# Kernel optimization log

Measured on AMD Instinct MI355X. Metric: run time of the kernel, lower is better.

## Reference

```python
import jax, jax.numpy as jnp
import numpy as np

B, S, D, DI = 8, 4096, 512, 2048
EPS = 1e-12  # torch F.normalize eps


def _l2norm(x):
    n = jnp.sqrt(jnp.sum(x * x, axis=-1, keepdims=True))
    return x / jnp.maximum(n, EPS)


def setup_inputs() -> dict:
    key = jax.random.key(0)
    ks = jax.random.split(key, 10)
    sd = 1.0 / np.sqrt(D)
    si = 1.0 / np.sqrt(DI)
    return {
        "x": jax.random.normal(ks[0], (B, S, D), jnp.float32),
        "wq": jax.random.uniform(ks[1], (D, DI), jnp.float32, -sd, sd),
        "wk": jax.random.uniform(ks[2], (D, DI), jnp.float32, -sd, sd),
        "wv": jax.random.uniform(ks[3], (D, DI), jnp.float32, -sd, sd),
        "wo": jax.random.uniform(ks[4], (DI, D), jnp.float32, -si, si),
        "w1": jax.random.uniform(ks[5], (D, DI), jnp.float32, -sd, sd),
        "b1": jax.random.uniform(ks[6], (DI,), jnp.float32, -sd, sd),
        "w2": jax.random.uniform(ks[7], (DI, D), jnp.float32, -si, si),
        "b2": jax.random.uniform(ks[8], (D,), jnp.float32, -si, si),
    }


def reference(x, wq, wk, wv, wo, w1, b1, w2, b2):
    # Hydra attention (linear): normalize(q) * sum_s(normalize(k)*v)
    q = _l2norm(jnp.einsum('bsd,de->bse', x, wq))
    k = _l2norm(jnp.einsum('bsd,de->bse', x, wk))
    v = jnp.einsum('bsd,de->bse', x, wv)
    kv = jnp.sum(k * v, axis=-2, keepdims=True)  # [B,1,DI]
    attn = jnp.einsum('bse,ed->bsd', q * kv, wo) + x  # dropout = identity (eval)
    # position-wise FFN with residual
    h = jax.nn.relu(jnp.einsum('bsd,de->bse', attn, w1) + b1)
    out = jnp.einsum('bse,ed->bsd', h, w2) + b2 + attn
    return out
```

## Files before the change

### kernel.cpp

```cpp
#include <hip/hip_runtime.h>
#include <stdint.h>

#define Bb  8
#define Ss  4096
#define Dd  512
#define DIi 2048
#define Mm  (Bb*Ss)

typedef unsigned short u16;
typedef __bf16 bf16x8 __attribute__((ext_vector_type(8)));
typedef float  f32x4  __attribute__((ext_vector_type(4)));

__device__ __forceinline__ float bfu(unsigned int u) {
  return __uint_as_float((u & 0xffffu) << 16);
}
__device__ __forceinline__ u16 f2bu(float f) {
  unsigned int x = __float_as_uint(f);
  return (u16)((x + 0x7fffu + ((x >> 16) & 1u)) >> 16);
}

__device__ __forceinline__ void tr_tile(const float* __restrict__ W, u16* __restrict__ Wt,
                                        int K, int N, int local, int tid) {
  __shared__ float t[32][33];
  const int nx = N / 32;
  const int n0 = (local % nx) * 32, k0 = (local / nx) * 32;
  const int tx = tid & 31, ty = tid >> 5;
#pragma unroll
  for (int i = 0; i < 32; i += 8)
    t[ty + i][tx] = W[(long)(k0 + ty + i) * N + n0 + tx];
  __syncthreads();
#pragma unroll
  for (int i = 0; i < 32; i += 8)
    Wt[(long)(n0 + ty + i) * K + k0 + tx] = f2bu(t[tx][ty + i]);
}

__global__ __launch_bounds__(256) void prep(
    const float* __restrict__ x, u16* __restrict__ xb,
    const float* wv, const float* w1, const float* wo, const float* w2,
    const float* wq, const float* wk,
    u16* wvT, u16* w1T, u16* woT, u16* w2T, u16* wqb, u16* wkb,
    float* __restrict__ zptr) {
  const int bid = blockIdx.x, tid = threadIdx.x;
  if (bid < 320) {
    zptr[bid * 256 + tid] = 0.f;
  } else if (bid < 2368) {
    long i = (long)(bid - 320) * 256 + tid;
    const long n4 = (long)Mm * Dd / 4;
    const long st = 2048L * 256;
    for (; i < n4; i += st) {
      float4 v = ((const float4*)x)[i];
      ushort4 o;
      o.x = f2bu(v.x); o.y = f2bu(v.y); o.z = f2bu(v.z); o.w = f2bu(v.w);
      ((ushort4*)xb)[i] = o;
    }
  } else if (bid < 3392)  tr_tile(wv, wvT, Dd, DIi, bid - 2368, tid);
  else if (bid < 4416)    tr_tile(w1, w1T, Dd, DIi, bid - 3392, tid);
  else if (bid < 5440)    tr_tile(wo, woT, DIi, Dd, bid - 4416, tid);
  else if (bid < 6464)    tr_tile(w2, w2T, DIi, Dd, bid - 5440, tid);
  else if (bid < 7488) {
    long i = (long)(bid - 6464) * 256 + tid;
    float4 v = ((const float4*)wq)[i];
    ushort4 o;
    o.x = f2bu(v.x); o.y = f2bu(v.y); o.z = f2bu(v.z); o.w = f2bu(v.w);
    ((ushort4*)wqb)[i] = o;
  } else {
    long i = (long)(bid - 7488) * 256 + tid;
    float4 v = ((const float4*)wk)[i];
    ushort4 o;
    o.x = f2bu(v.x); o.y = f2bu(v.y); o.z = f2bu(v.z); o.w = f2bu(v.w);
    ((ushort4*)wkb)[i] = o;
  }
}

__global__ __launch_bounds__(256) void build_wob(const u16* __restrict__ woT,
                                                 const float* __restrict__ kv,
                                                 u16* __restrict__ wob) {
  const int b = blockIdx.y;
  long i = (long)blockIdx.x * 256 + threadIdx.x;
  const long tot = (long)Dd * DIi / 8;
  if (i >= tot) return;
  const long e = i * 8;
  const int k = (int)(e & (DIi - 1));
  ushort4 w0 = *(const ushort4*)(woT + e);
  ushort4 w1 = *(const ushort4*)(woT + e + 4);
  const float* kvp = kv + (long)b * DIi + k;
  ushort4 o0, o1;
  o0.x = f2bu(bfu(w0.x) * kvp[0]); o0.y = f2bu(bfu(w0.y) * kvp[1]);
  o0.z = f2bu(bfu(w0.z) * kvp[2]); o0.w = f2bu(bfu(w0.w) * kvp[3]);
  o1.x = f2bu(bfu(w1.x) * kvp[4]); o1.y = f2bu(bfu(w1.y) * kvp[5]);
  o1.z = f2bu(bfu(w1.z) * kvp[6]); o1.w = f2bu(bfu(w1.w) * kvp[7]);
  u16* dst = wob + (long)b * Dd * DIi + e;
  *(ushort4*)dst = o0;
  *(ushort4*)(dst + 4) = o1;
}

__global__ void tr_x(const u16* __restrict__ xb, const float* __restrict__ nksq,
                     u16* __restrict__ xT, u16* __restrict__ xrnT) {
  __shared__ u16 t[32][33];
  __shared__ float rns[32];
  const int b = blockIdx.z;
  const int s0 = blockIdx.y * 32, d0 = blockIdx.x * 32;
  const int tx = threadIdx.x, ty = threadIdx.y;
  const size_t sbase = (size_t)b * Ss + s0;
#pragma unroll
  for (int i = 0; i < 32; i += 8)
    t[ty + i][tx] = xb[(sbase + ty + i) * Dd + d0 + tx];
  if (ty == 0) {
    const float nk = fmaxf(nksq[sbase + tx], 0.f);
    rns[tx] = 1.f / fmaxf(sqrtf(nk), 1e-12f);
  }
  __syncthreads();
  const size_t dbase = (size_t)b * Dd + d0;
#pragma unroll
  for (int i = 0; i < 32; i += 8) {
    const u16 v = t[tx][ty + i];
    const size_t idx = (dbase + ty + i) * Ss + s0 + tx;
    xT[idx] = v;
    xrnT[idx] = f2bu(bfu(v) * rns[tx]);
  }
}

__global__ __launch_bounds__(256) void colsum_kv(const u16* __restrict__ wkb,
                                                 const u16* __restrict__ Tb,
                                                 float* __restrict__ kv) {
  const int b = blockIdx.y;
  const int e = blockIdx.x * 256 + threadIdx.x;
  const int d0 = blockIdx.z * 64;
  const u16* wp = wkb + (size_t)d0 * DIi + e;
  const u16* tp = Tb + (size_t)b * Dd * DIi + (size_t)d0 * DIi + e;
  float a = 0.f;
#pragma unroll 4
  for (int d = 0; d < 64; ++d) {
    a += bfu(wp[0]) * bfu(tp[0]);
    wp += DIi; tp += DIi;
  }
  atomicAdd(&kv[(size_t)b * DIi + e], a);
}

#define GLL(src, dst) \
  __builtin_amdgcn_global_load_lds((const __attribute__((address_space(1))) unsigned int*)(src), \
                                   (__attribute__((address_space(3))) unsigned int*)(dst), 16, 0, 0)

enum { G_FFN1 = 2, G_FFN2 = 3 };

template<int MODE>
__global__ __launch_bounds__(512, 2) void gemm8(
    const u16* __restrict__ A, const u16* __restrict__ Bt,
    int N, int K,
    u16* __restrict__ Ybf, float* __restrict__ Yf,
    const u16* __restrict__ resb, const float* __restrict__ bias)
{
  __shared__ u16 lds8[65536];

  const int bx = blockIdx.x;
  const int by = blockIdx.y;
  const int tid  = threadIdx.x;
  const int lane = tid & 63;
  const int wid  = tid >> 6;
  const int wr = wid >> 2, wc = wid & 3;
  const int l15 = lane & 15, lg = lane >> 4;

  const long bm0 = (long)by * 256;
  const long bn0 = (long)bx * 256;
  const int NT = K >> 6;

  const u16* pA = A + bm0 * K;
  const u16* pB = Bt + bn0 * K;

  const int rowT = ((tid >> 6) << 3) | (tid & 7);
  const int cc8  = ((tid >> 3) & 7) * 8;

#define STAGE(PTR, LD, H, TT, BUFU, REGU) do {                                  \
    const u16* s0_ = (PTR) + (size_t)((H) * 128 + rowT) * (LD)                  \
                     + (size_t)(TT) * 64 + cc8;                                 \
    u16* d_ = lds8 + (BUFU) + (REGU) + (H) * 8192 + wid * 512;                  \
    GLL(s0_, d_);                                                               \
    GLL(s0_ + (size_t)64 * (LD), d_ + 4096);                                    \
  } while (0)

  const int aoff = (wr * 16384 + (l15 >> 3) * 1024 + lg * 128 + (l15 & 7) * 16) >> 1;
  const int boff = (32768 + (wc >> 1) * 16384 + (wc & 1) * 8192 +
                    (l15 >> 3) * 1024 + lg * 128 + (l15 & 7) * 16) >> 1;
#define LDA(M_, KS_, BU_) (*(const bf16x8*)(lds8 + (BU_) + aoff + (M_) * 1024 + (KS_) * 256))
#define LDB(N_, KS_, BU_) (*(const bf16x8*)(lds8 + (BU_) + boff + (N_) * 1024 + (KS_) * 256))

  f32x4 acc[8][4] = {};

  STAGE(pA, K, 0, 0, 0, 0);
  STAGE(pA, K, 1, 0, 0, 0);
  STAGE(pB, K, 0, 0, 0, 16384);
  STAGE(pB, K, 1, 0, 0, 16384);
  STAGE(pA, K, 0, 1, 32768, 0);
  asm volatile("s_waitcnt vmcnt(2)" ::: "memory");
  __builtin_amdgcn_s_barrier();

  for (int t = 0; t < NT; ++t) {
    const int bufu = (t & 1) * 32768;
    const int nbuf = bufu ^ 32768;
    bf16x8 aF[4], bF[4];

#pragma unroll
    for (int n = 0; n < 4; ++n) bF[n] = LDB(n, 0, bufu);
#pragma unroll
    for (int m = 0; m < 4; ++m) aF[m] = LDA(m, 0, bufu);
    if (t + 1 < NT) STAGE(pA, K, 1, t + 1, nbuf, 0);
    __builtin_amdgcn_s_barrier();
    __builtin_amdgcn_s_setprio(1);
#pragma unroll
    for (int m = 0; m < 4; ++m)
#pragma unroll
      for (int n = 0; n < 4; ++n)
        acc[m][n] = __builtin_amdgcn_mfma_f32_16x16x32_bf16(aF[m], bF[n], acc[m][n], 0, 0, 0);
    __builtin_amdgcn_s_setprio(0);

#pragma unroll
    for (int m = 0; m < 4; ++m) aF[m] = LDA(4 + m, 0, bufu);
    if (t + 1 < NT) STAGE(pB, K, 0, t + 1, nbuf, 16384);
    __builtin_amdgcn_s_barrier();
    __builtin_amdgcn_s_setprio(1);
#pragma unroll
    for (int m = 0; m < 4; ++m)
#pragma unroll
      for (int n = 0; n < 4; ++n)
        acc[4 + m][n] = __builtin_amdgcn_mfma_f32_16x16x32_bf16(aF[m], bF[n], acc[4 + m][n], 0, 0, 0);
    __builtin_amdgcn_s_setprio(0);

#pragma unroll
    for (int n = 0; n < 4; ++n) bF[n] = LDB(n, 1, bufu);
#pragma unroll
    for (int m = 0; m < 4; ++m) aF[m] = LDA(m, 1, bufu);
    if (t + 1 < NT) STAGE(pB, K, 1, t + 1, nbuf, 16384);
    __builtin_amdgcn_s_barrier();
    __builtin_amdgcn_s_setprio(1);
#pragma unroll
    for (int m = 0; m < 4; ++m)
#pragma unroll
      for (int n = 0; n < 4; ++n)
        acc[m][n] = __builtin_amdgcn_mfma_f32_16x16x32_bf16(aF[m], bF[n], acc[m][n], 0, 0, 0);
    __builtin_amdgcn_s_setprio(0);

#pragma unroll
    for (int m = 0; m < 4; ++m) aF[m] = LDA(4 + m, 1, bufu);
    __builtin_amdgcn_s_barrier();
    __builtin_amdgcn_s_setprio(1);
#pragma unroll
    for (int m = 0; m < 4; ++m)
#pragma unroll
      for (int n = 0; n < 4; ++n)
        acc[4 + m][n] = __builtin_amdgcn_mfma_f32_16x16x32_bf16(aF[m], bF[n], acc[4 + m][n], 0, 0, 0);
    __builtin_amdgcn_s_setprio(0);

    if (t + 1 < NT) {
      __builtin_amdgcn_s_barrier();
      if (t + 2 < NT) {
        STAGE(pA, K, 0, t + 2, bufu, 0);
        asm volatile("s_waitcnt vmcnt(2)" ::: "memory");
      } else {
        asm volatile("s_waitcnt vmcnt(0)" ::: "memory");
      }
      __builtin_amdgcn_s_barrier();
    }
  }

#pragma unroll
  for (int m = 0; m < 8; ++m) {
    const long row0 = bm0 + wr * 128 + m * 16 + lg * 4;
#pragma unroll
    for (int n = 0; n < 4; ++n) {
      const long col = bn0 + wc * 64 + n * 16 + l15;
#pragma unroll
      for (int r = 0; r < 4; ++r) {
        const long idx = (row0 + r) * N + col;
        const float v = acc[m][n][r];
        if constexpr (MODE == G_FFN1) {
          float o = v + bias[col];
          o = o > 0.f ? o : 0.f;
          Ybf[idx] = f2bu(o);
        } else {
          Yf[idx] = v + bias[col] + bfu(resb[idx]);
        }
      }
    }
  }
#undef STAGE
#undef LDA
#undef LDB
}

__global__ __launch_bounds__(256) void mega_small(
    const u16* __restrict__ wqb, const u16* __restrict__ wkb,
    const u16* __restrict__ wob,
    u16* __restrict__ Gt, u16* __restrict__ Gkt, u16* __restrict__ Ut, int zbase)
{
  __shared__ u16 As[4096];
  __shared__ u16 Bs[4096];
  const int K = DIi;
  const int idx = blockIdx.z + zbase;
  const u16* A  = (idx == 1) ? wkb : wqb;
  const u16* Bt = (idx == 0) ? wqb : (idx == 1) ? wkb
                  : wob + (size_t)(idx - 2) * Dd * DIi;
  u16* Ct = (idx == 0) ? Gt : (idx == 1) ? Gkt
            : Ut + (size_t)(idx - 2) * Dd * Dd;

  const int tid = threadIdx.x, lane = tid & 63, w = tid >> 6;
  const int wr = w >> 1, wc = w & 1;
  const int l15 = lane & 15, lg = lane >> 4;
  const long bm0 = (long)blockIdx.y * 128;
  const long bn0 = (long)blockIdx.x * 128;

  const int c0 = tid, c1 = tid + 256;
  const u16* aS0 = A  + (bm0 + (c0 >> 2)) * K + (c0 & 3) * 8;
  const u16* aS1 = A  + (bm0 + (c1 >> 2)) * K + (c1 & 3) * 8;
  const u16* bS0 = Bt + (bn0 + (c0 >> 2)) * K + (c0 & 3) * 8;
  const u16* bS1 = Bt + (bn0 + (c1 >> 2)) * K + (c1 & 3) * 8;
  u16* aD0 = As + w * 512;
  u16* aD1 = As + 2048 + w * 512;
  u16* bD0 = Bs + w * 512;
  u16* bD1 = Bs + 2048 + w * 512;

  f32x4 acc[4][4] = {};

  for (int k0 = 0; k0 < K; k0 += 32) {
    GLL(aS0 + k0, aD0);
    GLL(aS1 + k0, aD1);
    GLL(bS0 + k0, bD0);
    GLL(bS1 + k0, bD1);
    __syncthreads();
    bf16x8 af[4], bfv[4];
#pragma unroll
    for (int m = 0; m < 4; ++m)
      af[m] = *(const bf16x8*)(As + (wr * 64 + m * 16 + l15) * 32 + lg * 8);
#pragma unroll
    for (int n = 0; n < 4; ++n)
      bfv[n] = *(const bf16x8*)(Bs + (wc * 64 + n * 16 + l15) * 32 + lg * 8);
#pragma unroll
    for (int m = 0; m < 4; ++m)
#pragma unroll
      for (int n = 0; n < 4; ++n)
        acc[m][n] = __builtin_amdgcn_mfma_f32_16x16x32_bf16(af[m], bfv[n], acc[m][n], 0, 0, 0);
    __syncthreads();
  }

#pragma unroll
  for (int m = 0; m < 4; ++m) {
    const int row0 = (int)bm0 + wr * 64 + m * 16 + lg * 4;
#pragma unroll
    for (int n = 0; n < 4; ++n) {
      const int col = (int)bn0 + wc * 64 + n * 16 + l15;
      ushort4 o;
      o.x = f2bu(acc[m][n][0]); o.y = f2bu(acc[m][n][1]);
      o.z = f2bu(acc[m][n][2]); o.w = f2bu(acc[m][n][3]);
      *(ushort4*)(Ct + (size_t)col * Dd + row0) = o;
    }
  }
}

__global__ __launch_bounds__(256) void megacb(
    const u16* __restrict__ xrnT, const u16* __restrict__ xT,
    u16* __restrict__ Cb)
{
  __shared__ u16 As[2048];
  __shared__ u16 Bs[2048];
  const int K = Ss;
  const int z = blockIdx.z;
  const u16* A  = xrnT + (size_t)z * Dd * Ss;
  const u16* Bt = xT   + (size_t)z * Dd * Ss;
  u16* C = Cb + (size_t)z * Dd * Dd;

  const int tid = threadIdx.x, lane = tid & 63, w = tid >> 6;
  const int wr = w >> 1, wc = w & 1;
  const int l15 = lane & 15, lg = lane >> 4;
  const long bm0 = (long)blockIdx.y * 64;
  const long bn0 = (long)blockIdx.x * 64;

  const u16* aS0 = A  + (bm0 + (tid >> 2)) * K + (tid & 3) * 8;
  const u16* bS0 = Bt + (bn0 + (tid >> 2)) * K + (tid & 3) * 8;
  u16* aD0 = As + w * 512;
  u16* bD0 = Bs + w * 512;

  f32x4 acc[2][2] = {};

  for (int k0 = 0; k0 < K; k0 += 32) {
    GLL(aS0 + k0, aD0);
    GLL(bS0 + k0, bD0);
    __syncthreads();
    bf16x8 af[2], bfv[2];
#pragma unroll
    for (int m = 0; m < 2; ++m)
      af[m] = *(const bf16x8*)(As + (wr * 32 + m * 16 + l15) * 32 + lg * 8);
#pragma unroll
    for (int n = 0; n < 2; ++n)
      bfv[n] = *(const bf16x8*)(Bs + (wc * 32 + n * 16 + l15) * 32 + lg * 8);
#pragma unroll
    for (int m = 0; m < 2; ++m)
#pragma unroll
      for (int n = 0; n < 2; ++n)
        acc[m][n] = __builtin_amdgcn_mfma_f32_16x16x32_bf16(af[m], bfv[n], acc[m][n], 0, 0, 0);
    __syncthreads();
  }

#pragma unroll
  for (int m = 0; m < 2; ++m) {
    const long row0 = bm0 + wr * 32 + m * 16 + lg * 4;
#pragma unroll
    for (int n = 0; n < 2; ++n) {
      const long col = bn0 + wc * 32 + n * 16 + l15;
#pragma unroll
      for (int r = 0; r < 4; ++r)
        C[(row0 + r) * Dd + col] = f2bu(acc[m][n][r]);
    }
  }
}

__global__ __launch_bounds__(256) void megatb(
    const u16* __restrict__ Cb, const u16* __restrict__ wvT,
    u16* __restrict__ Tb)
{
  __shared__ u16 As[4096];
  __shared__ u16 Bs[4096];
  const int K = Dd, N = DIi;
  const int z = blockIdx.z;
  const u16* A  = Cb + (size_t)z * Dd * Dd;
  u16* C = Tb + (size_t)z * Dd * DIi;

  const int tid = threadIdx.x, lane = tid & 63, w = tid >> 6;
  const int wr = w >> 1, wc = w & 1;
  const int l15 = lane & 15, lg = lane >> 4;
  const long bm0 = (long)blockIdx.y * 128;
  const long bn0 = (long)blockIdx.x * 128;

  const int c0 = tid, c1 = tid + 256;
  const u16* aS0 = A   + (bm0 + (c0 >> 2)) * K + (c0 & 3) * 8;
  const u16* aS1 = A   + (bm0 + (c1 >> 2)) * K + (c1 & 3) * 8;
  const u16* bS0 = wvT + (bn0 + (c0 >> 2)) * K + (c0 & 3) * 8;
  const u16* bS1 = wvT + (bn0 + (c1 >> 2)) * K + (c1 & 3) * 8;
  u16* aD0 = As + w * 512;
  u16* aD1 = As + 2048 + w * 512;
  u16* bD0 = Bs + w * 512;
  u16* bD1 = Bs + 2048 + w * 512;

  f32x4 acc[4][4] = {};

  for (int k0 = 0; k0 < K; k0 += 32) {
    GLL(aS0 + k0, aD0);
    GLL(aS1 + k0, aD1);
    GLL(bS0 + k0, bD0);
    GLL(bS1 + k0, bD1);
    __syncthreads();
    bf16x8 af[4], bfv[4];
#pragma unroll
    for (int m = 0; m < 4; ++m)
      af[m] = *(const bf16x8*)(As + (wr * 64 + m * 16 + l15) * 32 + lg * 8);
#pragma unroll
    for (int n = 0; n < 4; ++n)
      bfv[n] = *(const bf16x8*)(Bs + (wc * 64 + n * 16 + l15) * 32 + lg * 8);
#pragma unroll
    for (int m = 0; m < 4; ++m)
#pragma unroll
      for (int n = 0; n < 4; ++n)
        acc[m][n] = __builtin_amdgcn_mfma_f32_16x16x32_bf16(af[m], bfv[n], acc[m][n], 0, 0, 0);
    __syncthreads();
  }

#pragma unroll
  for (int m = 0; m < 4; ++m) {
    const long row0 = bm0 + wr * 64 + m * 16 + lg * 4;
#pragma unroll
    for (int n = 0; n < 4; ++n) {
      const long col = bn0 + wc * 64 + n * 16 + l15;
#pragma unroll
      for (int r = 0; r < 4; ++r)
        C[(row0 + r) * N + col] = f2bu(acc[m][n][r]);
    }
  }
}

template<int MODE>
__global__ __launch_bounds__(256) void mega_nx(
    const u16* __restrict__ xb, const u16* __restrict__ Gt, const u16* __restrict__ Gkt,
    const u16* __restrict__ Ut,
    float* __restrict__ nqsq, float* __restrict__ nksq, u16* __restrict__ attnb)
{
  __shared__ u16 As[4096];
  __shared__ u16 Bs[4096];
  __shared__ u16 xs[16384];
  const int K = Dd, N = Dd;

  const int tid = threadIdx.x, lane = tid & 63, w = tid >> 6;
  const int wr = w >> 1, wc = w & 1;
  const int l15 = lane & 15, lg = lane >> 4;
  const bool isK = (MODE == 0) && (blockIdx.y >= Mm / 128);
  const long bm0 = (long)(isK ? blockIdx.y - Mm / 128 : blockIdx.y) * 128;
  const long bn0 = (long)blockIdx.x * 128;
  const int bq = (int)(bm0 >> 12);
  const u16* Bt = (MODE == 0) ? (isK ? Gkt : Gt) : Ut + (size_t)bq * Dd * Dd;
  float* nsq = (MODE == 0) ? (isK ? nksq : nqsq) : nqsq;

  const int c0 = tid, c1 = tid + 256;
  const u16* aS0 = xb + (bm0 + (c0 >> 2)) * K + (c0 & 3) * 8;
  const u16* aS1 = xb + (bm0 + (c1 >> 2)) * K + (c1 & 3) * 8;
  const u16* bS0 = Bt + (bn0 + (c0 >> 2)) * K + (c0 & 3) * 8;
  const u16* bS1 = Bt + (bn0 + (c1 >> 2)) * K + (c1 & 3) * 8;
  u16* aD0 = As + w * 512;
  u16* aD1 = As + 2048 + w * 512;
  u16* bD0 = Bs + w * 512;
  u16* bD1 = Bs + 2048 + w * 512;

  f32x4 acc[4][4] = {};

  for (int k0 = 0; k0 < K; k0 += 32) {
    GLL(aS0 + k0, aD0);
    GLL(aS1 + k0, aD1);
    GLL(bS0 + k0, bD0);
    GLL(bS1 + k0, bD1);
    __syncthreads();
    bf16x8 af[4], bfv[4];
#pragma unroll
    for (int m = 0; m < 4; ++m)
      af[m] = *(const bf16x8*)(As + (wr * 64 + m * 16 + l15) * 32 + lg * 8);
#pragma unroll
    for (int n = 0; n < 4; ++n)
      bfv[n] = *(const bf16x8*)(Bs + (wc * 64 + n * 16 + l15) * 32 + lg * 8);
#pragma unroll
    for (int m = 0; m < 4; ++m)
#pragma unroll
      for (int n = 0; n < 4; ++n)
        acc[m][n] = __builtin_amdgcn_mfma_f32_16x16x32_bf16(af[m], bfv[n], acc[m][n], 0, 0, 0);
    __syncthreads();
  }

#pragma unroll
  for (int i = 0; i < 8; ++i) {
    const int c = i * 256 + tid;
    const int rowL = c >> 4;
    const int srcslot = (c & 15) ^ (rowL & 15);
    const u16* src = xb + (size_t)(bm0 + rowL) * Dd + bn0 + srcslot * 8;
    GLL(src, xs + i * 2048 + w * 512);
  }
  asm volatile("s_waitcnt vmcnt(0)" ::: "memory");
  __builtin_amdgcn_s_barrier();

#define XV(RL, CL) bfu(xs[(RL) * 128 + ((((CL) >> 3) ^ ((RL) & 15)) << 3) + ((CL) & 7)])

  if constexpr (MODE == 0) {
    float sk[16];
#pragma unroll
    for (int i = 0; i < 16; ++i) sk[i] = 0.f;
#pragma unroll
    for (int m = 0; m < 4; ++m) {
#pragma unroll
      for (int n = 0; n < 4; ++n) {
        const int colL = wc * 64 + n * 16 + l15;
#pragma unroll
        for (int r = 0; r < 4; ++r) {
          const int rowL = wr * 64 + m * 16 + lg * 4 + r;
          sk[m * 4 + r] += acc[m][n][r] * XV(rowL, colL);
        }
      }
    }
#pragma unroll
    for (int i = 0; i < 16; ++i) {
#pragma unroll
      for (int off = 1; off < 16; off <<= 1)
        sk[i] += __shfl_xor(sk[i], off, 64);
    }
    if (l15 == 0) {
#pragma unroll
      for (int m = 0; m < 4; ++m)
#pragma unroll
        for (int r = 0; r < 4; ++r)
          atomicAdd(&nsq[bm0 + wr * 64 + m * 16 + lg * 4 + r], sk[m * 4 + r]);
    }
  } else {
#pragma unroll
    for (int m = 0; m < 4; ++m) {
      const long row0 = bm0 + wr * 64 + m * 16 + lg * 4;
      float rq[4];
#pragma unroll
      for (int r = 0; r < 4; ++r)
        rq[r] = 1.f / fmaxf(sqrtf(fmaxf(nqsq[row0 + r], 0.f)), 1e-12f);
#pragma unroll
      for (int n = 0; n < 4; ++n) {
        const int colL = wc * 64 + n * 16 + l15;
#pragma unroll
        for (int r = 0; r < 4; ++r) {
          const int rowL = wr * 64 + m * 16 + lg * 4 + r;
          attnb[(row0 + r) * N + bn0 + colL] = f2bu(acc[m][n][r] * rq[r] + XV(rowL, colL));
        }
      }
    }
  }
#undef XV
}

extern "C" void kernel_launch(void* const* d_in, const int* in_sizes, int n_in,
                              void* d_out, int out_size, void* d_ws, size_t ws_size,
                              hipStream_t stream) {
  const float* x  = (const float*)d_in[0];
  const float* wq = (const float*)d_in[1];
  const float* wk = (const float*)d_in[2];
  const float* wv = (const float*)d_in[3];
  const float* wo = (const float*)d_in[4];
  const float* w1 = (const float*)d_in[5];
  const float* b1 = (const float*)d_in[6];
  const float* w2 = (const float*)d_in[7];
  const float* b2 = (const float*)d_in[8];
  float* out = (float*)d_out;

  char* p = (char*)d_ws;
  auto take = [&](size_t bytes) {
    char* r = p; p += (bytes + 255) & ~(size_t)255; return r;
  };
  u16*   xb    = (u16*)take((size_t)Mm * Dd * 2);
  u16*   wvT   = (u16*)take((size_t)DIi * Dd * 2);
  u16*   w1T   = (u16*)take((size_t)DIi * Dd * 2);
  u16*   woT   = (u16*)take((size_t)Dd * DIi * 2);
  u16*   w2T   = (u16*)take((size_t)Dd * DIi * 2);
  u16*   wqb   = (u16*)take((size_t)Dd * DIi * 2);
  u16*   wkb   = (u16*)take((size_t)Dd * DIi * 2);
  u16*   Gt    = (u16*)take((size_t)Dd * Dd * 2);
  u16*   Gkt   = (u16*)take((size_t)Dd * Dd * 2);
  u16*   Ut    = (u16*)take((size_t)Bb * Dd * Dd * 2);
  u16*   buf1  = (u16*)take((size_t)Mm * DIi * 2);
  u16*   attnb = (u16*)take((size_t)Mm * Dd * 2);
  float* nksq  = (float*)take((size_t)Mm * 4);
  float* nqsq  = (float*)take((size_t)Mm * 4);
  float* kvp   = (float*)take((size_t)Bb * DIi * 4);
  u16* xT   = buf1;
  u16* xrnT = buf1 + (size_t)Mm * Dd;
  u16* Tb   = buf1 + 2 * (size_t)Mm * Dd;
  u16* Cb   = buf1 + 2 * (size_t)Mm * Dd + (size_t)Bb * Dd * DIi;
  u16* wob  = buf1 + 2 * (size_t)Mm * Dd + (size_t)Bb * Dd * DIi
                   + (size_t)Bb * Dd * Dd;
  (void)in_sizes; (void)n_in; (void)out_size; (void)ws_size;

  prep<<<8512, 256, 0, stream>>>(x, xb, wv, w1, wo, w2, wq, wk,
                                 wvT, w1T, woT, w2T, wqb, wkb, nksq);

  mega_small<<<dim3(4, 4, 2), 256, 0, stream>>>(wqb, wkb, nullptr, Gt, Gkt, Ut, 0);

  mega_nx<0><<<dim3(4, 2 * Mm / 128), 256, 0, stream>>>(
      xb, Gt, Gkt, nullptr, nqsq, nksq, nullptr);

  tr_x<<<dim3(Dd / 32, Ss / 32, Bb), dim3(32, 8), 0, stream>>>(xb, nksq, xT, xrnT);

  megacb<<<dim3(8, 8, Bb), 256, 0, stream>>>(xrnT, xT, Cb);

  megatb<<<dim3(16, 4, Bb), 256, 0, stream>>>(Cb, wvT, Tb);

  colsum_kv<<<dim3(8, Bb, 8), 256, 0, stream>>>(wkb, Tb, kvp);

  build_wob<<<dim3(512, Bb), 256, 0, stream>>>(woT, kvp, wob);

  mega_small<<<dim3(4, 4, 8), 256, 0, stream>>>(wqb, wkb, wob, Gt, Gkt, Ut, 2);

  mega_nx<1><<<dim3(4, Mm / 128), 256, 0, stream>>>(
      xb, nullptr, nullptr, Ut, nqsq, nullptr, attnb);

  gemm8<G_FFN1><<<dim3(DIi / 256, Mm / 256), 512, 0, stream>>>(
      attnb, w1T, DIi, Dd, buf1, nullptr, nullptr, b1);

  gemm8<G_FFN2><<<dim3(Dd / 256, Mm / 256), 512, 0, stream>>>(
      buf1, w2T, Dd, DIi, nullptr, out, attnb, b2);
}
```

Measured before the change: 475.1 us.

## Fuse kv column-sum into megatb epilogue and merge q/k norm GEMMs

The megatb GEMM no longer writes the bf16 T tensor. Its epilogue instead multiplies the accumulators by wk and reduces across rows, atomically adding straight into kv, which removes the separate colsum_kv kernel and the T round trip through memory. The q and k norm-square GEMMs are also merged into one kernel, mega_nxg, that shares the x tile loads across two B operands and two accumulator sets. In exchange, register pressure and LDS use go up in the merged kernel, kv now depends on more atomics, and kv no longer sees T's bf16 rounding.

```diff
diff --git a/kernel.cpp b/kernel.cpp
--- a/kernel.cpp
+++ b/kernel.cpp
@@ -120,23 +120,6 @@
   }
 }
 
-__global__ __launch_bounds__(256) void colsum_kv(const u16* __restrict__ wkb,
-                                                 const u16* __restrict__ Tb,
-                                                 float* __restrict__ kv) {
-  const int b = blockIdx.y;
-  const int e = blockIdx.x * 256 + threadIdx.x;
-  const int d0 = blockIdx.z * 64;
-  const u16* wp = wkb + (size_t)d0 * DIi + e;
-  const u16* tp = Tb + (size_t)b * Dd * DIi + (size_t)d0 * DIi + e;
-  float a = 0.f;
-#pragma unroll 4
-  for (int d = 0; d < 64; ++d) {
-    a += bfu(wp[0]) * bfu(tp[0]);
-    wp += DIi; tp += DIi;
-  }
-  atomicAdd(&kv[(size_t)b * DIi + e], a);
-}
-
 #define GLL(src, dst) \
   __builtin_amdgcn_global_load_lds((const __attribute__((address_space(1))) unsigned int*)(src), \
                                    (__attribute__((address_space(3))) unsigned int*)(dst), 16, 0, 0)
@@ -414,14 +397,13 @@
 
 __global__ __launch_bounds__(256) void megatb(
     const u16* __restrict__ Cb, const u16* __restrict__ wvT,
-    u16* __restrict__ Tb)
+    const u16* __restrict__ wkb, float* __restrict__ kv)
 {
   __shared__ u16 As[4096];
   __shared__ u16 Bs[4096];
-  const int K = Dd, N = DIi;
+  const int K = Dd;
   const int z = blockIdx.z;
-  const u16* A  = Cb + (size_t)z * Dd * Dd;
-  u16* C = Tb + (size_t)z * Dd * DIi;
+  const u16* A = Cb + (size_t)z * Dd * Dd;
 
   const int tid = threadIdx.x, lane = tid & 63, w = tid >> 6;
   const int wr = w >> 1, wc = w & 1;
@@ -462,24 +444,146 @@
     __syncthreads();
   }
 
+  float cs[4] = {0.f, 0.f, 0.f, 0.f};
 #pragma unroll
   for (int m = 0; m < 4; ++m) {
-    const long row0 = bm0 + wr * 64 + m * 16 + lg * 4;
+    const long drow0 = bm0 + wr * 64 + m * 16 + lg * 4;
 #pragma unroll
     for (int n = 0; n < 4; ++n) {
       const long col = bn0 + wc * 64 + n * 16 + l15;
 #pragma unroll
       for (int r = 0; r < 4; ++r)
-        C[(row0 + r) * N + col] = f2bu(acc[m][n][r]);
-    }
-  }
-}
-
-template<int MODE>
-__global__ __launch_bounds__(256) void mega_nx(
+        cs[n] += bfu(wkb[(drow0 + r) * DIi + col]) * acc[m][n][r];
+    }
+  }
+#pragma unroll
+  for (int n = 0; n < 4; ++n) {
+    cs[n] += __shfl_xor(cs[n], 16, 64);
+    cs[n] += __shfl_xor(cs[n], 32, 64);
+  }
+  if (lane < 16) {
+#pragma unroll
+    for (int n = 0; n < 4; ++n) {
+      const long col = bn0 + wc * 64 + n * 16 + l15;
+      atomicAdd(&kv[(size_t)z * DIi + col], cs[n]);
+    }
+  }
+}
+
+__global__ __launch_bounds__(256) void mega_nxg(
     const u16* __restrict__ xb, const u16* __restrict__ Gt, const u16* __restrict__ Gkt,
-    const u16* __restrict__ Ut,
-    float* __restrict__ nqsq, float* __restrict__ nksq, u16* __restrict__ attnb)
+    float* __restrict__ nqsq, float* __restrict__ nksq)
+{
+  __shared__ u16 As[4096];
+  __shared__ u16 Bs1[4096];
+  __shared__ u16 Bs2[4096];
+  __shared__ u16 xs[16384];
+  const int K = Dd;
+
+  const int tid = threadIdx.x, lane = tid & 63, w = tid >> 6;
+  const int wr = w >> 1, wc = w & 1;
+  const int l15 = lane & 15, lg = lane >> 4;
+  const long bm0 = (long)blockIdx.y * 128;
+  const long bn0 = (long)blockIdx.x * 128;
+
+  const int c0 = tid, c1 = tid + 256;
+  const u16* aS0 = xb  + (bm0 + (c0 >> 2)) * K + (c0 & 3) * 8;
+  const u16* aS1 = xb  + (bm0 + (c1 >> 2)) * K + (c1 & 3) * 8;
+  const u16* b1S0 = Gt  + (bn0 + (c0 >> 2)) * K + (c0 & 3) * 8;
+  const u16* b1S1 = Gt  + (bn0 + (c1 >> 2)) * K + (c1 & 3) * 8;
+  const u16* b2S0 = Gkt + (bn0 + (c0 >> 2)) * K + (c0 & 3) * 8;
+  const u16* b2S1 = Gkt + (bn0 + (c1 >> 2)) * K + (c1 & 3) * 8;
+  u16* aD0 = As + w * 512;
+  u16* aD1 = As + 2048 + w * 512;
+  u16* b1D0 = Bs1 + w * 512;
+  u16* b1D1 = Bs1 + 2048 + w * 512;
+  u16* b2D0 = Bs2 + w * 512;
+  u16* b2D1 = Bs2 + 2048 + w * 512;
+
+  f32x4 acc1[4][4] = {};
+  f32x4 acc2[4][4] = {};
+
+  for (int k0 = 0; k0 < K; k0 += 32) {
+    GLL(aS0 + k0, aD0);
+    GLL(aS1 + k0, aD1);
+    GLL(b1S0 + k0, b1D0);
+    GLL(b1S1 + k0, b1D1);
+    GLL(b2S0 + k0, b2D0);
+    GLL(b2S1 + k0, b2D1);
+    __syncthreads();
+    bf16x8 af[4], bf1[4], bf2[4];
+#pragma unroll
+    for (int m = 0; m < 4; ++m)
+      af[m] = *(const bf16x8*)(As + (wr * 64 + m * 16 + l15) * 32 + lg * 8);
+#pragma unroll
+    for (int n = 0; n < 4; ++n) {
+      bf1[n] = *(const bf16x8*)(Bs1 + (wc * 64 + n * 16 + l15) * 32 + lg * 8);
+      bf2[n] = *(const bf16x8*)(Bs2 + (wc * 64 + n * 16 + l15) * 32 + lg * 8);
+    }
+#pragma unroll
+    for (int m = 0; m < 4; ++m)
+#pragma unroll
+      for (int n = 0; n < 4; ++n) {
+        acc1[m][n] = __builtin_amdgcn_mfma_f32_16x16x32_bf16(af[m], bf1[n], acc1[m][n], 0, 0, 0);
+        acc2[m][n] = __builtin_amdgcn_mfma_f32_16x16x32_bf16(af[m], bf2[n], acc2[m][n], 0, 0, 0);
+      }
+    __syncthreads();
+  }
+
+#pragma unroll
+  for (int i = 0; i < 8; ++i) {
+    const int c = i * 256 + tid;
+    const int rowL = c >> 4;
+    const int srcslot = (c & 15) ^ (rowL & 15);
+    const u16* src = xb + (size_t)(bm0 + rowL) * Dd + bn0 + srcslot * 8;
+    GLL(src, xs + i * 2048 + w * 512);
+  }
+  asm volatile("s_waitcnt vmcnt(0)" ::: "memory");
+  __builtin_amdgcn_s_barrier();
+
+#define XV(RL, CL) bfu(xs[(RL) * 128 + ((((CL) >> 3) ^ ((RL) & 15)) << 3) + ((CL) & 7)])
+
+  float s1[16], s2[16];
+#pragma unroll
+  for (int i = 0; i < 16; ++i) { s1[i] = 0.f; s2[i] = 0.f; }
+#pragma unroll
+  for (int m = 0; m < 4; ++m) {
+#pragma unroll
+    for (int n = 0; n < 4; ++n) {
+      const int colL = wc * 64 + n * 16 + l15;
+#pragma unroll
+      for (int r = 0; r < 4; ++r) {
+        const int rowL = wr * 64 + m * 16 + lg * 4 + r;
+        const float xv = XV(rowL, colL);
+        s1[m * 4 + r] += acc1[m][n][r] * xv;
+        s2[m * 4 + r] += acc2[m][n][r] * xv;
+      }
+    }
+  }
+#pragma unroll
+  for (int i = 0; i < 16; ++i) {
+#pragma unroll
+    for (int off = 1; off < 16; off <<= 1) {
+      s1[i] += __shfl_xor(s1[i], off, 64);
+      s2[i] += __shfl_xor(s2[i], off, 64);
+    }
+  }
+  if (l15 == 0) {
+#pragma unroll
+    for (int m = 0; m < 4; ++m)
+#pragma unroll
+      for (int r = 0; r < 4; ++r) {
+        const long row = bm0 + wr * 64 + m * 16 + lg * 4 + r;
+        atomicAdd(&nqsq[row], s1[m * 4 + r]);
+        atomicAdd(&nksq[row], s2[m * 4 + r]);
+      }
+  }
+#undef XV
+}
+
+__global__ __launch_bounds__(256) void mega_awo(
+    const u16* __restrict__ xb, const u16* __restrict__ Ut,
+    const float* __restrict__ nqsq, u16* __restrict__ attnb)
 {
   __shared__ u16 As[4096];
   __shared__ u16 Bs[4096];
@@ -489,12 +593,10 @@
   const int tid = threadIdx.x, lane = tid & 63, w = tid >> 6;
   const int wr = w >> 1, wc = w & 1;
   const int l15 = lane & 15, lg = lane >> 4;
-  const bool isK = (MODE == 0) && (blockIdx.y >= Mm / 128);
-  const long bm0 = (long)(isK ? blockIdx.y - Mm / 128 : blockIdx.y) * 128;
+  const long bm0 = (long)blockIdx.y * 128;
   const long bn0 = (long)blockIdx.x * 128;
   const int bq = (int)(bm0 >> 12);
-  const u16* Bt = (MODE == 0) ? (isK ? Gkt : Gt) : Ut + (size_t)bq * Dd * Dd;
-  float* nsq = (MODE == 0) ? (isK ? nksq : nqsq) : nqsq;
+  const u16* Bt = Ut + (size_t)bq * Dd * Dd;
 
   const int c0 = tid, c1 = tid + 256;
   const u16* aS0 = xb + (bm0 + (c0 >> 2)) * K + (c0 & 3) * 8;
@@ -542,51 +644,20 @@
 
 #define XV(RL, CL) bfu(xs[(RL) * 128 + ((((CL) >> 3) ^ ((RL) & 15)) << 3) + ((CL) & 7)])
 
-  if constexpr (MODE == 0) {
-    float sk[16];
-#pragma unroll
-    for (int i = 0; i < 16; ++i) sk[i] = 0.f;
-#pragma unroll
-    for (int m = 0; m < 4; ++m) {
-#pragma unroll
-      for (int n = 0; n < 4; ++n) {
-        const int colL = wc * 64 + n * 16 + l15;
-#pragma unroll
-        for (int r = 0; r < 4; ++r) {
-          const int rowL = wr * 64 + m * 16 + lg * 4 + r;
-          sk[m * 4 + r] += acc[m][n][r] * XV(rowL, colL);
-        }
-      }
-    }
-#pragma unroll
-    for (int i = 0; i < 16; ++i) {
-#pragma unroll
-      for (int off = 1; off < 16; off <<= 1)
-        sk[i] += __shfl_xor(sk[i], off, 64);
-    }
-    if (l15 == 0) {
-#pragma unroll
-      for (int m = 0; m < 4; ++m)
-#pragma unroll
-        for (int r = 0; r < 4; ++r)
-          atomicAdd(&nsq[bm0 + wr * 64 + m * 16 + lg * 4 + r], sk[m * 4 + r]);
-    }
-  } else {
-#pragma unroll
-    for (int m = 0; m < 4; ++m) {
-      const long row0 = bm0 + wr * 64 + m * 16 + lg * 4;
-      float rq[4];
-#pragma unroll
-      for (int r = 0; r < 4; ++r)
-        rq[r] = 1.f / fmaxf(sqrtf(fmaxf(nqsq[row0 + r], 0.f)), 1e-12f);
-#pragma unroll
-      for (int n = 0; n < 4; ++n) {
-        const int colL = wc * 64 + n * 16 + l15;
-#pragma unroll
-        for (int r = 0; r < 4; ++r) {
-          const int rowL = wr * 64 + m * 16 + lg * 4 + r;
-          attnb[(row0 + r) * N + bn0 + colL] = f2bu(acc[m][n][r] * rq[r] + XV(rowL, colL));
-        }
+#pragma unroll
+  for (int m = 0; m < 4; ++m) {
+    const long row0 = bm0 + wr * 64 + m * 16 + lg * 4;
+    float rq[4];
+#pragma unroll
+    for (int r = 0; r < 4; ++r)
+      rq[r] = 1.f / fmaxf(sqrtf(fmaxf(nqsq[row0 + r], 0.f)), 1e-12f);
+#pragma unroll
+    for (int n = 0; n < 4; ++n) {
+      const int colL = wc * 64 + n * 16 + l15;
+#pragma unroll
+      for (int r = 0; r < 4; ++r) {
+        const int rowL = wr * 64 + m * 16 + lg * 4 + r;
+        attnb[(row0 + r) * N + bn0 + colL] = f2bu(acc[m][n][r] * rq[r] + XV(rowL, colL));
       }
     }
   }
@@ -628,10 +699,8 @@
   float* kvp   = (float*)take((size_t)Bb * DIi * 4);
   u16* xT   = buf1;
   u16* xrnT = buf1 + (size_t)Mm * Dd;
-  u16* Tb   = buf1 + 2 * (size_t)Mm * Dd;
-  u16* Cb   = buf1 + 2 * (size_t)Mm * Dd + (size_t)Bb * Dd * DIi;
-  u16* wob  = buf1 + 2 * (size_t)Mm * Dd + (size_t)Bb * Dd * DIi
-                   + (size_t)Bb * Dd * Dd;
+  u16* Cb   = buf1 + 2 * (size_t)Mm * Dd;
+  u16* wob  = buf1 + 2 * (size_t)Mm * Dd + (size_t)Bb * Dd * Dd;
   (void)in_sizes; (void)n_in; (void)out_size; (void)ws_size;
 
   prep<<<8512, 256, 0, stream>>>(x, xb, wv, w1, wo, w2, wq, wk,
@@ -639,23 +708,19 @@
 
   mega_small<<<dim3(4, 4, 2), 256, 0, stream>>>(wqb, wkb, nullptr, Gt, Gkt, Ut, 0);
 
-  mega_nx<0><<<dim3(4, 2 * Mm / 128), 256, 0, stream>>>(
-      xb, Gt, Gkt, nullptr, nqsq, nksq, nullptr);
+  mega_nxg<<<dim3(4, Mm / 128), 256, 0, stream>>>(xb, Gt, Gkt, nqsq, nksq);
 
   tr_x<<<dim3(Dd / 32, Ss / 32, Bb), dim3(32, 8), 0, stream>>>(xb, nksq, xT, xrnT);
 
   megacb<<<dim3(8, 8, Bb), 256, 0, stream>>>(xrnT, xT, Cb);
 
-  megatb<<<dim3(16, 4, Bb), 256, 0, stream>>>(Cb, wvT, Tb);
-
-  colsum_kv<<<dim3(8, Bb, 8), 256, 0, stream>>>(wkb, Tb, kvp);
+  megatb<<<dim3(16, 4, Bb), 256, 0, stream>>>(Cb, wvT, wkb, kvp);
 
   build_wob<<<dim3(512, Bb), 256, 0, stream>>>(woT, kvp, wob);
 
   mega_small<<<dim3(4, 4, 8), 256, 0, stream>>>(wqb, wkb, wob, Gt, Gkt, Ut, 2);
 
-  mega_nx<1><<<dim3(4, Mm / 128), 256, 0, stream>>>(
-      xb, nullptr, nullptr, Ut, nqsq, nullptr, attnb);
+  mega_awo<<<dim3(4, Mm / 128), 256, 0, stream>>>(xb, Ut, nqsq, attnb);
 
   gemm8<G_FFN1><<<dim3(DIi / 256, Mm / 256), 512, 0, stream>>>(
       attnb, w1T, DIi, Dd, buf1, nullptr, nullptr, b1);
```

After: 496.3 us. 1.04x slower.
